# Optimization experiments

Measured on AMD Instinct MI355X. Metric: run time of the kernel, lower is better.

The kernel has to match this reference:

```python
import jax, jax.numpy as jnp
import numpy as np
from jax import lax

BN_EPS = 1e-5
TINY = 1e-12


def conv2d(x, w, stride, padding):
    # NCHW x OIHW -> NCHW
    return lax.conv_general_dilated(
        x, w, (stride, stride), [(padding, padding), (padding, padding)],
        dimension_numbers=('NCHW', 'OIHW', 'NCHW'))


def pool2x2(x):
    B, C, H, W = x.shape
    return x.reshape(B, C, H // 2, 2, W // 2, 2).mean(axis=(3, 5))


def setup_inputs() -> dict:
    key = jax.random.key(0)
    k0, k1, k2, k3 = jax.random.split(key, 4)
    B, Cin, H, W = 32, 128, 56, 56
    Cout, K = 256, 3
    mean = jax.random.normal(k0, (B, Cin, H, W), jnp.float32)
    std = jax.random.uniform(k1, (B, Cin, H, W), jnp.float32)  # std must be >= 0
    fan_in = Cin * K * K
    bound = 1.0 / np.sqrt(fan_in)  # torch Conv2d default init
    conv_w = jax.random.uniform(k2, (Cout, Cin, K, K), jnp.float32, -bound, bound)
    conv_b = jax.random.uniform(k3, (Cout,), jnp.float32, -bound, bound)
    bn_gamma = jnp.full((Cout,), 2.5, jnp.float32)  # module fills weight with 2.5
    bn_beta = jnp.full((Cout,), 2.5, jnp.float32)   # module fills bias with 2.5
    return {'mean': mean, 'std': std, 'conv_w': conv_w, 'conv_b': conv_b,
            'bn_gamma': bn_gamma, 'bn_beta': bn_beta}


def reference(mean, std, conv_w, conv_b, bn_gamma, bn_beta):
    # mean branch: standard conv
    m = conv2d(mean, conv_w, 1, 1) + conv_b[None, :, None, None]
    # std branch (no rho): independent-variance propagation, var -> conv with w^2
    var = conv2d(std * std, conv_w * conv_w, 1, 1)
    s = jnp.sqrt(var + TINY)
    # BatchNorm2d in training mode: batch statistics over (N, H, W)
    mu = jnp.mean(m, axis=(0, 2, 3), keepdims=True)
    v = jnp.var(m, axis=(0, 2, 3), keepdims=True)  # biased, like torch normalization
    inv = 1.0 / jnp.sqrt(v + BN_EPS)
    g = bn_gamma[None, :, None, None]
    uhat = (m - mu) * inv * g + bn_beta[None, :, None, None]
    # std through BN: pure linear scale by |gamma| / sqrt(var + eps)
    shat = s * inv * jnp.abs(g)
    # moment activation (erf-based Gaussian->Heaviside moment mapping)
    z = uhat / (shat * np.sqrt(2.0) + TINY)
    u = 0.5 * (1.0 + lax.erf(z))               # output mean in (0, 1)
    sa = jnp.sqrt(jnp.clip(u * (1.0 - u), TINY))  # output std of Bernoulli-like moments
    # avg-pool 2x2 stride 2: mean pools linearly, independent vars: std = sqrt(avg(var))/2
    u_p = pool2x2(u)
    s_p = jnp.sqrt(pool2x2(sa * sa)) * 0.5
    return (u_p, s_p)
```

## Files before the change

### kernel.cpp

```cpp
#include <hip/hip_runtime.h>
#include <hip/hip_bf16.h>
#include <math.h>

#define BB 32
#define CIN 128
#define HH 56
#define WW 56
#define COUT 256
#define HW (HH*WW)
#define NPIX (BB*HW)
#define PH 28
#define PW 28
#define POOL_ELEMS ((long)BB*COUT*PH*PW)
#define PADH 58
#define PADW 58
#define ROW_BLOCKS (BB*HH)
#define TOPBOT_BLOCKS (BB*2)
#define WPACK_BLOCKS ((9*COUT*CIN)/256)

typedef unsigned short u16;
using s16x8 = __attribute__((ext_vector_type(8))) short;
using s16x4 = __attribute__((ext_vector_type(4))) short;
using f32x4 = __attribute__((ext_vector_type(4))) float;

__device__ __forceinline__ float b2f(u16 u){ return __uint_as_float(((unsigned)u)<<16); }
__device__ __forceinline__ u16 f2b(float x){
    unsigned u = __float_as_uint(x);
    unsigned r = (u + 0x7fffu + ((u>>16)&1u)) >> 16;
    return (u16)r;
}

__device__ __forceinline__ void gload16(const void* g, void* l){
    __builtin_amdgcn_global_load_lds(
        (const __attribute__((address_space(1))) unsigned int*)g,
        (__attribute__((address_space(3))) unsigned int*)l, 16, 0, 0);
}


__global__ __launch_bounds__(256) void prep_kernel(
    const float* __restrict__ mean, const float* __restrict__ stdv,
    const float* __restrict__ w,
    u16* __restrict__ mean_pad, u16* __restrict__ std2_pad,
    u16* __restrict__ BP, u16* __restrict__ BP2,
    float* __restrict__ sum_, float* __restrict__ sumsq_)
{
    const int bid = blockIdx.x;
    const int t   = threadIdx.x;

    if (bid < ROW_BLOCKS){
        __shared__ u16 ldsm[56*128];
        __shared__ u16 ldss[56*128];
        const int b = bid / HH;
        const int h = bid - b*HH;

        #pragma unroll
        for (int k=0; k<7; ++k){
            int idx = k*256 + t;
            int c   = idx / 14;
            int f4  = idx - c*14;
            long ga = ((long)(b*CIN + c)*HH + h)*WW + f4*4;
            const f32x4 m4 = *(const f32x4*)(mean + ga);
            const f32x4 s4 = *(const f32x4*)(stdv + ga);
            #pragma unroll
            for (int j=0; j<4; ++j){
                int px = f4*4 + j;
                int ci = px*128 + (c ^ ((px & 15) << 3));
                ldsm[ci] = f2b(m4[j]);
                ldss[ci] = f2b(s4[j] * s4[j]);
            }
        }
        __syncthreads();

        const long rowbase = ((long)(b*PADH + (h+1)))*PADW*CIN;
        #pragma unroll
        for (int k=0; k<4; ++k){
            int slot = k*256 + t;
            int px   = slot >> 4;
            int oct  = slot & 15;
            if (px < 56){
                int ci = px*128 + ((oct ^ (px & 15)) << 3);
                long o = rowbase + (long)(px+1)*CIN + oct*8;
                *(s16x8*)(mean_pad + o) = *(const s16x8*)&ldsm[ci];
                *(s16x8*)(std2_pad + o) = *(const s16x8*)&ldss[ci];
            }
        }
        if (t < 64){
            int buf = t >> 5;
            int ppx = ((t >> 4) & 1) ? 57 : 0;
            int oct = t & 15;
            long o  = rowbase + (long)ppx*CIN + oct*8;
            s16x8 z = (s16x8){0,0,0,0,0,0,0,0};
            *(s16x8*)((buf ? std2_pad : mean_pad) + o) = z;
        }
    } else if (bid < ROW_BLOCKS + TOPBOT_BLOCKS){
        int row = bid - ROW_BLOCKS;
        int b   = row >> 1;
        int ph  = (row & 1) ? (PADH-1) : 0;
        const long rowbase = ((long)(b*PADH + ph))*PADW*CIN;
        s16x8 z = (s16x8){0,0,0,0,0,0,0,0};
        #pragma unroll
        for (int k=0; k<8; ++k){
            int g = k*256 + t;
            if (g < 2*PADW*16){
                int buf = g >= PADW*16;
                int gg  = buf ? g - PADW*16 : g;
                int px  = gg >> 4;
                int oct = gg & 15;
                long o  = rowbase + (long)px*CIN + oct*8;
                *(s16x8*)((buf ? std2_pad : mean_pad) + o) = z;
            }
        }
        if (row == 0){ sum_[t] = 0.f; sumsq_[t] = 0.f; }
    } else {
        int tt = (bid - ROW_BLOCKS - TOPBOT_BLOCKS)*256 + t;
        int e    = tt & 7;
        int co   = (tt >> 3) & 255;
        int rest = tt >> 11;
        int ks   = rest >> 2;
        int sub  = rest & 3;
        int r    = ks >> 2;
        int ci   = (ks & 3)*32 + sub*8 + e;
        float v = w[((long)co*CIN + ci)*9 + r];
        BP[tt]  = f2b(v);
        BP2[tt] = f2b(v*v);
    }
}

__global__ __launch_bounds__(512,4) void convw_kernel(
    const u16* __restrict__ mean_pad, const u16* __restrict__ std2_pad,
    const u16* __restrict__ BP, const u16* __restrict__ BP2,
    const float* __restrict__ bias,
    u16* __restrict__ m_out, u16* __restrict__ v_out,
    float* __restrict__ sum_, float* __restrict__ sumsq_)
{
    __shared__ u16 lds[33024];
    const int tid  = threadIdx.x;
    const int lane = tid & 63;
    const int wv   = tid >> 6;

    int gid   = blockIdx.x;
    int local = gid >> 3;
    int p     = (gid & 7)*112 + (local >> 1);
    int path  = local & 1;
    const int b  = p / 28;
    const int h0 = (p - b*28) * 2;

    const u16* __restrict__ Ap = path ? std2_pad : mean_pad;
    const u16* __restrict__ Bp = path ? BP2      : BP;
    u16*       __restrict__ Op = path ? v_out    : m_out;

    const int slot_g = (tid & 15) ^ ((tid >> 4) & 15);
    const int wbase  = (b*PADH + h0)*PADW*CIN;
    const int athr   = (tid >> 4)*CIN + slot_g*8;
    #pragma unroll
    for (int i=0; i<8; ++i){
        const int Ci = (i>>1)*(PADW*CIN) + (i&1)*32*CIN;
        gload16(Ap + wbase + Ci + athr, &lds[i*4096 + tid*8]);
    }
    __syncthreads();

    const int q = lane >> 4;

    const u16* bp = Bp + (size_t)((lane>>4)*256 + wv*32 + (lane&15))*8;

    f32x4 acc[8][2];
    #pragma unroll
    for (int i=0;i<8;i++){ acc[i][0] = (f32x4){0,0,0,0}; acc[i][1] = (f32x4){0,0,0,0}; }

    #pragma unroll
    for (int r=0; r<9; ++r){
        const int kh = r/3, kw = r - (r/3)*3;

        int ab[8];
        #pragma unroll
        for (int mi=0; mi<8; ++mi){
            int R   = (mi>>2)*64 + (mi&3)*16 + (lane & 15) + kh*64 + kw;
            int t15 = ((lane & 15) + kw) & 15;
            ab[mi] = R*128 + ((q ^ t15) << 3);
        }

        #pragma unroll
        for (int hf=0; hf<2; ++hf){
            #pragma unroll
            for (int kk=0; kk<2; ++kk){
                const size_t ksoff = (size_t)(r*4 + hf*2 + kk)*8192;
                s16x8 bf0 = *(const s16x8*)(bp + ksoff);
                s16x8 bf1 = *(const s16x8*)(bp + ksoff + 128);
                const int sx = hf*64 + kk*32;
                s16x8 af[8];
                #pragma unroll
                for (int mi=0; mi<8; ++mi)
                    af[mi] = *(const s16x8*)&lds[ab[mi] ^ sx];
                __builtin_amdgcn_s_setprio(1);
                #pragma unroll
                for (int mi=0; mi<8; ++mi){
                    acc[mi][0] = __builtin_amdgcn_mfma_f32_16x16x32_bf16(af[mi], bf0, acc[mi][0], 0,0,0);
                    acc[mi][1] = __builtin_amdgcn_mfma_f32_16x16x32_bf16(af[mi], bf1, acc[mi][1], 0,0,0);
                }
                __builtin_amdgcn_s_setprio(0);
            }
        }
    }

    float bv[2];
    if (path == 0){
        bv[0] = bias[wv*32 + (lane&15)];
        bv[1] = bias[wv*32 + 16 + (lane&15)];
    } else {
        bv[0] = 0.f; bv[1] = 0.f;
    }

    float ssum[2] = {0.f,0.f}, ssq[2] = {0.f,0.f};

    #pragma unroll
    for (int mi=0; mi<8; ++mi){
        int dh = mi >> 2;
        int w  = (mi&3)*16 + ((lane>>4)<<2);
        if (w < 56){
            #pragma unroll
            for (int ni=0; ni<2; ++ni){
                int co = wv*32 + ni*16 + (lane&15);
                size_t o = (size_t)(b*COUT + co)*HW + (size_t)(h0+dh)*WW + w;
                s16x4 pk;
                #pragma unroll
                for (int rr=0; rr<4; ++rr){
                    float vv = acc[mi][ni][rr] + bv[ni];
                    pk[rr] = (short)f2b(vv);
                    ssum[ni] += vv;
                    ssq[ni]  += vv*vv;
                }
                *(s16x4*)(Op + o) = pk;
            }
        }
    }

    if (path == 0){
        #pragma unroll
        for (int ni=0; ni<2; ++ni){
            float s = ssum[ni], s2 = ssq[ni];
            s  += __shfl_xor(s, 16, 64);  s2 += __shfl_xor(s2, 16, 64);
            s  += __shfl_xor(s, 32, 64);  s2 += __shfl_xor(s2, 32, 64);
            if (lane < 16){
                int co = wv*32 + ni*16 + lane;
                atomicAdd(&sum_[co],   s);
                atomicAdd(&sumsq_[co], s2);
            }
        }
    }
}

__global__ __launch_bounds__(256) void final_kernel(
        const u16* __restrict__ m, const u16* __restrict__ var,
        const float* __restrict__ sum_, const float* __restrict__ sumsq_,
        const float* __restrict__ gamma, const float* __restrict__ beta,
        float* __restrict__ out){
    int idx4 = blockIdx.x*256 + threadIdx.x;
    int wo4 = idx4 % (PW/4); int t = idx4 / (PW/4);
    int ho = t % PH; t /= PH;
    int co = t % COUT; int b = t / COUT;
    float g  = gamma[co];
    float be = beta[co];
    float mu = sum_[co] / (float)NPIX;
    float vr = sumsq_[co] / (float)NPIX - mu*mu;
    float inv = 1.0f / sqrtf(vr + 1e-5f);
    float ag = fabsf(g);
    float us[4] = {0.f,0.f,0.f,0.f}, ss[4] = {0.f,0.f,0.f,0.f};
    #pragma unroll
    for (int dh=0; dh<2; ++dh){
        long base = ((long)(b*COUT+co)*HH + 2*ho+dh)*WW + wo4*8;
        const s16x8 vm = *(const s16x8*)&m[base];
        const s16x8 vv = *(const s16x8*)&var[base];
        #pragma unroll
        for (int j=0;j<8;j++){
            float mm = b2f((u16)vm[j]);
            float sdev = sqrtf(b2f((u16)vv[j]) + 1e-12f);
            float uhat = (mm - mu)*inv*g + be;
            float shat = sdev*inv*ag;
            float z = uhat / (shat*1.41421356237f + 1e-12f);
            float u = 0.5f*(1.f + erff(z));
            us[j>>1] += u;
            ss[j>>1] += fmaxf(u*(1.f-u), 1e-12f);
        }
    }
    long ob = ((long)(b*COUT+co)*PH + ho)*PW + wo4*4;
    f32x4 o0, o1;
    #pragma unroll
    for (int k=0;k<4;k++){
        o0[k] = 0.25f*us[k];
        o1[k] = sqrtf(0.25f*ss[k])*0.5f;
    }
    *(f32x4*)(out + ob) = o0;
    *(f32x4*)(out + POOL_ELEMS + ob) = o1;
}


__global__ void wtransf_kernel(const float* __restrict__ w, float* __restrict__ wT){
    int out = blockIdx.x*256 + threadIdx.x;
    if (out >= COUT*CIN*9) return;
    int co = out % COUT;
    int r  = out / COUT;
    wT[out] = w[(long)co*(CIN*9) + r];
}

__global__ __launch_bounds__(256) void stats_old_kernel(const u16* __restrict__ m,
        float* __restrict__ mu_out, float* __restrict__ inv_out){
    int co = blockIdx.x;
    float s=0.f, s2=0.f;
    for (int oc = threadIdx.x; oc < NPIX/8; oc += 256){
        int b = oc / (HW/8); int o8 = oc - b*(HW/8);
        const s16x8 v8 = *(const s16x8*)&m[((size_t)(b*COUT+co))*HW + (size_t)o8*8];
        #pragma unroll
        for (int j=0;j<8;j++){ float v = b2f((u16)v8[j]); s += v; s2 += v*v; }
    }
    __shared__ float rs[256], rs2[256];
    rs[threadIdx.x]=s; rs2[threadIdx.x]=s2; __syncthreads();
    for (int o=128;o>0;o>>=1){
        if (threadIdx.x < o){ rs[threadIdx.x]+=rs[threadIdx.x+o]; rs2[threadIdx.x]+=rs2[threadIdx.x+o]; }
        __syncthreads();
    }
    if (threadIdx.x==0){
        float mu = rs[0]/(float)NPIX;
        float var = rs2[0]/(float)NPIX - mu*mu;
        mu_out[co] = mu;
        inv_out[co] = 1.0f/sqrtf(var + 1e-5f);
    }
}

__global__ __launch_bounds__(256) void final_old_kernel(
        const u16* __restrict__ m, const u16* __restrict__ var,
        const float* __restrict__ mu_, const float* __restrict__ inv_,
        const float* __restrict__ gamma, const float* __restrict__ beta,
        float* __restrict__ out){
    long idx = (long)blockIdx.x*256 + threadIdx.x;
    int wo = (int)(idx % PW); long t = idx / PW;
    int ho = (int)(t % PH); t /= PH;
    int co = (int)(t % COUT); int b = (int)(t / COUT);
    float g  = gamma[co];
    float be = beta[co];
    float mu = mu_[co], inv = inv_[co];
    float ag = fabsf(g);
    float us = 0.f, ss = 0.f;
    #pragma unroll
    for (int dh=0; dh<2; ++dh){
        int hpos = 2*ho+dh;
        long base = ((long)(b*COUT+co)*HH + hpos)*WW + 2*wo;
        #pragma unroll
        for (int dw=0; dw<2; ++dw){
            float mm = b2f(m[base+dw]);
            float vv = b2f(var[base+dw]);
            float sdev = sqrtf(vv + 1e-12f);
            float uhat = (mm - mu)*inv*g + be;
            float shat = sdev*inv*ag;
            float z = uhat / (shat*1.41421356237f + 1e-12f);
            float u = 0.5f*(1.f + erff(z));
            float sa2 = fmaxf(u*(1.f-u), 1e-12f);
            us += u; ss += sa2;
        }
    }
    out[idx]              = 0.25f*us;
    out[POOL_ELEMS + idx] = sqrtf(0.25f*ss)*0.5f;
}

#define CI_CHUNK 64
#define XW 32
__global__ __launch_bounds__(256) void conv_old_kernel(
    const float* __restrict__ mean, const float* __restrict__ stdv,
    const float* __restrict__ wT, const float* __restrict__ bias,
    u16* __restrict__ m_out, u16* __restrict__ v_out)
{
    __shared__ float lds_m[CI_CHUNK][3][XW];
    __shared__ float lds_s[CI_CHUNK][3][XW];
    const int co   = threadIdx.x;
    const int half = blockIdx.x;
    const int h    = blockIdx.y;
    const int b    = blockIdx.z;
    const int w_base = half*28;

    float acc_m[28], acc_v[28];
    #pragma unroll
    for (int i=0;i<28;i++){ acc_m[i]=0.f; acc_v[i]=0.f; }

    for (int c=0; c<CIN; c+=CI_CHUNK){
        for (int t = threadIdx.x; t < CI_CHUNK*3*30; t += 256){
            int pos = t % 30; int r = t / 30; int hh = r % 3; int ci_l = r / 3;
            int gh = h - 1 + hh; int gw = w_base - 1 + pos;
            float vm = 0.f, vs = 0.f;
            if ((unsigned)gh < (unsigned)HH && (unsigned)gw < (unsigned)WW){
                long gi = ((long)(b*CIN + (c+ci_l))*HH + gh)*WW + gw;
                vm = mean[gi];
                float sv = stdv[gi];
                vs = sv*sv;
            }
            lds_m[ci_l][hh][pos] = vm;
            lds_s[ci_l][hh][pos] = vs;
        }
        __syncthreads();
        for (int ci_l=0; ci_l<CI_CHUNK; ++ci_l){
            int rbase = (c+ci_l)*9;
            #pragma unroll
            for (int kh=0; kh<3; ++kh){
                float w0 = wT[(long)(rbase + kh*3 + 0)*COUT + co];
                float w1 = wT[(long)(rbase + kh*3 + 1)*COUT + co];
                float w2 = wT[(long)(rbase + kh*3 + 2)*COUT + co];
                float xm[30];
                #pragma unroll
                for (int p=0;p<30;p++) xm[p] = lds_m[ci_l][kh][p];
                #pragma unroll
                for (int i=0;i<28;i++) acc_m[i] += w0*xm[i] + w1*xm[i+1] + w2*xm[i+2];
                float q0=w0*w0, q1=w1*w1, q2=w2*w2;
                float xs[30];
                #pragma unroll
                for (int p=0;p<30;p++) xs[p] = lds_s[ci_l][kh][p];
                #pragma unroll
                for (int i=0;i<28;i++) acc_v[i] += q0*xs[i] + q1*xs[i+1] + q2*xs[i+2];
            }
        }
        __syncthreads();
    }
    float bvv = bias[co];
    long obase = ((long)(b*COUT+co)*HH + h)*WW + w_base;
    #pragma unroll
    for (int i=0;i<28;i++){
        m_out[obase+i] = f2b(acc_m[i]+bvv);
        v_out[obase+i] = f2b(acc_v[i]);
    }
}

extern "C" void kernel_launch(void* const* d_in, const int* in_sizes, int n_in,
                              void* d_out, int out_size, void* d_ws, size_t ws_size,
                              hipStream_t stream)
{
    const float* mean   = (const float*)d_in[0];
    const float* stdv   = (const float*)d_in[1];
    const float* conv_w = (const float*)d_in[2];
    const float* conv_b = (const float*)d_in[3];
    const float* gamma  = (const float*)d_in[4];
    const float* beta   = (const float*)d_in[5];
    float* out = (float*)d_out;
    char* ws = (char*)d_ws;

    const size_t PAD_BYTES  = (size_t)BB*PADH*PADW*CIN*2;
    const size_t SLACK      = 8192;
    const size_t OFF_STD2   = PAD_BYTES + SLACK;
    const size_t OFF_WT     = OFF_STD2 + PAD_BYTES + SLACK;
    const size_t WT_BYTES   = (size_t)9*COUT*CIN*2;
    const size_t OFF_WT2    = OFF_WT + WT_BYTES;
    const size_t OFF_M      = OFF_WT2 + WT_BYTES;
    const size_t MV_BYTES   = (size_t)BB*COUT*HW*2;
    const size_t OFF_V      = OFF_M + MV_BYTES;
    const size_t OFF_SUM    = OFF_V + MV_BYTES;
    const size_t OFF_SUMSQ  = OFF_SUM + 1024;
    const size_t NEED_FAST  = OFF_SUMSQ + 1024;

    if (ws_size >= NEED_FAST){
        u16* mean_pad = (u16*)ws;
        u16* std2_pad = (u16*)(ws + OFF_STD2);
        u16* BP   = (u16*)(ws + OFF_WT);
        u16* BP2  = (u16*)(ws + OFF_WT2);
        u16* m_buf = (u16*)(ws + OFF_M);
        u16* v_buf = (u16*)(ws + OFF_V);
        float* sum_   = (float*)(ws + OFF_SUM);
        float* sumsq_ = (float*)(ws + OFF_SUMSQ);

        prep_kernel<<<ROW_BLOCKS + TOPBOT_BLOCKS + WPACK_BLOCKS, 256, 0, stream>>>(
            mean, stdv, conv_w, mean_pad, std2_pad, BP, BP2, sum_, sumsq_);
        convw_kernel<<<(NPIX/112)*2, 512, 0, stream>>>(
            mean_pad, std2_pad, BP, BP2, conv_b, m_buf, v_buf, sum_, sumsq_);
        final_kernel<<<(int)(POOL_ELEMS/4/256), 256, 0, stream>>>(
            m_buf, v_buf, sum_, sumsq_, gamma, beta, out);
    } else {
        u16* m_buf = (u16*)ws;
        u16* v_buf = (u16*)(ws + (size_t)BB*COUT*HW*2);
        float* wT  = (float*)(ws + (size_t)BB*COUT*HW*4);
        float* mu  = (float*)(ws + (size_t)BB*COUT*HW*4 + (size_t)COUT*CIN*9*4);
        float* inv = mu + 256;
        wtransf_kernel<<<(COUT*CIN*9+255)/256, 256, 0, stream>>>(conv_w, wT);
        conv_old_kernel<<<dim3(2, HH, BB), 256, 0, stream>>>(mean, stdv, wT, conv_b, m_buf, v_buf);
        stats_old_kernel<<<COUT, 256, 0, stream>>>(m_buf, mu, inv);
        final_old_kernel<<<(int)(POOL_ELEMS/256), 256, 0, stream>>>(m_buf, v_buf, mu, inv, gamma, beta, out);
    }
}
```

Baseline: 237.7 us.

## Switch conv MFMA from 16x16x32 to 32x32x16 tiles with padded output stride

The implicit-GEMM conv now uses 32x32x16 bf16 MFMA with four 32x32 accumulator tiles per wave instead of sixteen 16x16 tiles, and the weight packing layout is reordered to match. The output m/v buffers get a row stride of 64 so each 32-wide fragment can be stored without a bounds check, and the BN stats mask out the padding columns. The aim is fewer MFMA and LDS fragment loads per FLOP and simpler epilogue stores, at the cost of extra memory for the padded buffers and writes to columns nobody reads.

```diff
diff --git a/kernel.cpp b/kernel.cpp
--- a/kernel.cpp
+++ b/kernel.cpp
@@ -14,14 +14,16 @@
 #define POOL_ELEMS ((long)BB*COUT*PH*PW)
 #define PADH 58
 #define PADW 58
+#define MSTRIDE 64
 #define ROW_BLOCKS (BB*HH)
 #define TOPBOT_BLOCKS (BB*2)
 #define WPACK_BLOCKS ((9*COUT*CIN)/256)
 
 typedef unsigned short u16;
-using s16x8 = __attribute__((ext_vector_type(8))) short;
-using s16x4 = __attribute__((ext_vector_type(4))) short;
-using f32x4 = __attribute__((ext_vector_type(4))) float;
+using s16x8  = __attribute__((ext_vector_type(8)))  short;
+using s16x4  = __attribute__((ext_vector_type(4)))  short;
+using f32x4  = __attribute__((ext_vector_type(4)))  float;
+using f32x16 = __attribute__((ext_vector_type(16))) float;
 
 __device__ __forceinline__ float b2f(u16 u){ return __uint_as_float(((unsigned)u)<<16); }
 __device__ __forceinline__ u16 f2b(float x){
@@ -52,7 +54,6 @@
         __shared__ u16 ldss[56*128];
         const int b = bid / HH;
         const int h = bid - b*HH;
-
         #pragma unroll
         for (int k=0; k<7; ++k){
             int idx = k*256 + t;
@@ -70,7 +71,6 @@
             }
         }
         __syncthreads();
-
         const long rowbase = ((long)(b*PADH + (h+1)))*PADW*CIN;
         #pragma unroll
         for (int k=0; k<4; ++k){
@@ -113,13 +113,12 @@
         if (row == 0){ sum_[t] = 0.f; sumsq_[t] = 0.f; }
     } else {
         int tt = (bid - ROW_BLOCKS - TOPBOT_BLOCKS)*256 + t;
-        int e    = tt & 7;
-        int co   = (tt >> 3) & 255;
-        int rest = tt >> 11;
-        int ks   = rest >> 2;
-        int sub  = rest & 3;
-        int r    = ks >> 2;
-        int ci   = (ks & 3)*32 + sub*8 + e;
+        int e  = tt & 7;
+        int co = (tt >> 3) & 255;
+        int kq = (tt >> 11) & 1;
+        int s  = (tt >> 12) & 7;
+        int r  = tt >> 15;
+        int ci = s*16 + kq*8 + e;
         float v = w[((long)co*CIN + ci)*9 + r];
         BP[tt]  = f2b(v);
         BP2[tt] = f2b(v*v);
@@ -159,92 +158,75 @@
     }
     __syncthreads();
 
-    const int q = lane >> 4;
-
-    const u16* bp = Bp + (size_t)((lane>>4)*256 + wv*32 + (lane&15))*8;
-
-    f32x4 acc[8][2];
-    #pragma unroll
-    for (int i=0;i<8;i++){ acc[i][0] = (f32x4){0,0,0,0}; acc[i][1] = (f32x4){0,0,0,0}; }
+    const int l31 = lane & 31;
+    const int kq  = lane >> 5;
+
+    const u16* bpl = Bp + (size_t)(kq*2048 + (wv*32 + l31)*8);
+
+    f32x16 acc[4];
+    #pragma unroll
+    for (int f=0; f<4; ++f)
+      #pragma unroll
+      for (int e=0; e<16; ++e) acc[f][e] = 0.f;
 
     #pragma unroll
     for (int r=0; r<9; ++r){
         const int kh = r/3, kw = r - (r/3)*3;
 
-        int ab[8];
-        #pragma unroll
-        for (int mi=0; mi<8; ++mi){
-            int R   = (mi>>2)*64 + (mi&3)*16 + (lane & 15) + kh*64 + kw;
-            int t15 = ((lane & 15) + kw) & 15;
-            ab[mi] = R*128 + ((q ^ t15) << 3);
-        }
-
-        #pragma unroll
-        for (int hf=0; hf<2; ++hf){
+        int rowoff[4], t15[4];
+        #pragma unroll
+        for (int f=0; f<4; ++f){
+            int R = (f>>1)*64 + (f&1)*32 + l31 + kh*64 + kw;
+            rowoff[f] = R*128;
+            t15[f]    = R & 15;
+        }
+
+        #pragma unroll
+        for (int s=0; s<8; ++s){
+            s16x8 bf = *(const s16x8*)(bpl + (size_t)(r*8 + s)*4096);
+            s16x8 af[4];
             #pragma unroll
-            for (int kk=0; kk<2; ++kk){
-                const size_t ksoff = (size_t)(r*4 + hf*2 + kk)*8192;
-                s16x8 bf0 = *(const s16x8*)(bp + ksoff);
-                s16x8 bf1 = *(const s16x8*)(bp + ksoff + 128);
-                const int sx = hf*64 + kk*32;
-                s16x8 af[8];
-                #pragma unroll
-                for (int mi=0; mi<8; ++mi)
-                    af[mi] = *(const s16x8*)&lds[ab[mi] ^ sx];
-                __builtin_amdgcn_s_setprio(1);
-                #pragma unroll
-                for (int mi=0; mi<8; ++mi){
-                    acc[mi][0] = __builtin_amdgcn_mfma_f32_16x16x32_bf16(af[mi], bf0, acc[mi][0], 0,0,0);
-                    acc[mi][1] = __builtin_amdgcn_mfma_f32_16x16x32_bf16(af[mi], bf1, acc[mi][1], 0,0,0);
-                }
-                __builtin_amdgcn_s_setprio(0);
-            }
-        }
-    }
-
-    float bv[2];
+            for (int f=0; f<4; ++f){
+                int slot = (s*2 + kq) ^ t15[f];
+                af[f] = *(const s16x8*)&lds[rowoff[f] + (slot << 3)];
+            }
+            __builtin_amdgcn_s_setprio(1);
+            #pragma unroll
+            for (int f=0; f<4; ++f)
+                acc[f] = __builtin_amdgcn_mfma_f32_32x32x16_bf16(af[f], bf, acc[f], 0,0,0);
+            __builtin_amdgcn_s_setprio(0);
+        }
+    }
+
+    const int co = wv*32 + l31;
+    const float bv = (path == 0) ? bias[co] : 0.f;
+
+    float ssum = 0.f, ssq = 0.f;
+
+    #pragma unroll
+    for (int f=0; f<4; ++f){
+        const int fr = f>>1, fc = f&1;
+        const size_t obase = ((size_t)(b*COUT + co)*HH + (h0+fr))*MSTRIDE;
+        #pragma unroll
+        for (int g=0; g<4; ++g){
+            int w0 = fc*32 + g*8 + 4*kq;
+            s16x4 pk;
+            #pragma unroll
+            for (int rr=0; rr<4; ++rr){
+                float vv = acc[f][g*4+rr] + bv;
+                pk[rr] = (short)f2b(vv);
+                if (w0 + rr < 56){ ssum += vv; ssq += vv*vv; }
+            }
+            *(s16x4*)(Op + obase + w0) = pk;
+        }
+    }
+
     if (path == 0){
-        bv[0] = bias[wv*32 + (lane&15)];
-        bv[1] = bias[wv*32 + 16 + (lane&15)];
-    } else {
-        bv[0] = 0.f; bv[1] = 0.f;
-    }
-
-    float ssum[2] = {0.f,0.f}, ssq[2] = {0.f,0.f};
-
-    #pragma unroll
-    for (int mi=0; mi<8; ++mi){
-        int dh = mi >> 2;
-        int w  = (mi&3)*16 + ((lane>>4)<<2);
-        if (w < 56){
-            #pragma unroll
-            for (int ni=0; ni<2; ++ni){
-                int co = wv*32 + ni*16 + (lane&15);
-                size_t o = (size_t)(b*COUT + co)*HW + (size_t)(h0+dh)*WW + w;
-                s16x4 pk;
-                #pragma unroll
-                for (int rr=0; rr<4; ++rr){
-                    float vv = acc[mi][ni][rr] + bv[ni];
-                    pk[rr] = (short)f2b(vv);
-                    ssum[ni] += vv;
-                    ssq[ni]  += vv*vv;
-                }
-                *(s16x4*)(Op + o) = pk;
-            }
-        }
-    }
-
-    if (path == 0){
-        #pragma unroll
-        for (int ni=0; ni<2; ++ni){
-            float s = ssum[ni], s2 = ssq[ni];
-            s  += __shfl_xor(s, 16, 64);  s2 += __shfl_xor(s2, 16, 64);
-            s  += __shfl_xor(s, 32, 64);  s2 += __shfl_xor(s2, 32, 64);
-            if (lane < 16){
-                int co = wv*32 + ni*16 + lane;
-                atomicAdd(&sum_[co],   s);
-                atomicAdd(&sumsq_[co], s2);
-            }
+        ssum += __shfl_xor(ssum, 32, 64);
+        ssq  += __shfl_xor(ssq,  32, 64);
+        if (lane < 32){
+            atomicAdd(&sum_[wv*32 + lane],   ssum);
+            atomicAdd(&sumsq_[wv*32 + lane], ssq);
         }
     }
 }
@@ -267,7 +249,7 @@
     float us[4] = {0.f,0.f,0.f,0.f}, ss[4] = {0.f,0.f,0.f,0.f};
     #pragma unroll
     for (int dh=0; dh<2; ++dh){
-        long base = ((long)(b*COUT+co)*HH + 2*ho+dh)*WW + wo4*8;
+        long base = ((long)(b*COUT+co)*HH + 2*ho+dh)*MSTRIDE + wo4*8;
         const s16x8 vm = *(const s16x8*)&m[base];
         const s16x8 vv = *(const s16x8*)&var[base];
         #pragma unroll
@@ -446,7 +428,7 @@
     const size_t WT_BYTES   = (size_t)9*COUT*CIN*2;
     const size_t OFF_WT2    = OFF_WT + WT_BYTES;
     const size_t OFF_M      = OFF_WT2 + WT_BYTES;
-    const size_t MV_BYTES   = (size_t)BB*COUT*HW*2;
+    const size_t MV_BYTES   = (size_t)BB*COUT*HH*MSTRIDE*2;
     const size_t OFF_V      = OFF_M + MV_BYTES;
     const size_t OFF_SUM    = OFF_V + MV_BYTES;
     const size_t OFF_SUMSQ  = OFF_SUM + 1024;
```

Result: no change. 239.5 us (+0.7%).
